# Optimization experiments

Measured on AMD Instinct MI355X. Metric: run time of the kernel, lower is better.

## Reference

```python
import jax, jax.numpy as jnp
import numpy as np

HEADS = 8
DIM_HEAD = 64
EPS_NORM = 1e-5

def chan_layer_norm(x, g, b):
    # normalize over channel dim (axis=1), biased variance, eps inside sqrt
    mean = jnp.mean(x, axis=1, keepdims=True)
    var = jnp.mean((x - mean) ** 2, axis=1, keepdims=True)
    return (x - mean) / jnp.sqrt(var + EPS_NORM) * g + b

def l2norm(x):
    # F.normalize over dim=1 with eps=1e-12
    n = jnp.linalg.norm(x, axis=1, keepdims=True)
    return x / jnp.maximum(n, 1e-12)

def conv1x1(w, x):
    # w: (out_c, in_c), x: (b, in_c, h, w)
    return jnp.einsum('oc,bchw->bohw', w, x)

def setup_inputs() -> dict:
    key = jax.random.key(0)
    ks = jax.random.split(key, 8)
    dim, inner = 256, HEADS * DIM_HEAD
    B, H, W = 8, 64, 64
    inp = {
        'query_source': jax.random.normal(ks[0], (B, dim, H, W), jnp.float32),
        'context': jax.random.normal(ks[1], (B, dim, H, W), jnp.float32),
        'cn_g': jnp.ones((1, dim, 1, 1), jnp.float32),
        'cn_b': jnp.zeros((1, dim, 1, 1), jnp.float32),
        'qn_g': jnp.ones((1, dim, 1, 1), jnp.float32),
        'qn_b': jnp.zeros((1, dim, 1, 1), jnp.float32),
        'on_g': jnp.ones((1, dim, 1, 1), jnp.float32),
        'on_b': jnp.zeros((1, dim, 1, 1), jnp.float32),
        'w_kv': jax.random.normal(ks[2], (inner * 2, dim), jnp.float32) * (dim ** -0.5),
        'w_q': jax.random.normal(ks[3], (inner, dim), jnp.float32) * (dim ** -0.5),
        'w_out': jax.random.normal(ks[4], (dim, inner), jnp.float32) * (inner ** -0.5),
        'gamma': jnp.full((1,), 0.5, jnp.float32),  # nonzero so output depends on attention path
    }
    return inp

def reference(query_source, context, cn_g, cn_b, qn_g, qn_b, on_g, on_b, w_kv, w_q, w_out, gamma):
    B, C, Hq, Wq = query_source.shape
    _, _, Hc, Wc = context.shape
    kh = int(Hc ** 0.5)  # height_top_k default
    kw = int(Wc ** 0.5)  # width_top_k default

    ctx = chan_layer_norm(context, cn_g, cn_b)
    qs = chan_layer_norm(query_source, qn_g, qn_b)

    kv = conv1x1(w_kv, ctx)                      # (B, 2*inner, Hc, Wc)
    k, v = jnp.split(kv, 2, axis=1)
    q = conv1x1(w_q, qs)                         # (B, inner, Hq, Wq)

    def fold(x):
        b, hc, h, w = x.shape
        return x.reshape(b, HEADS, DIM_HEAD, h, w).reshape(b * HEADS, DIM_HEAD, h, w)
    q, k, v = fold(q), fold(k), fold(v)

    q, k = l2norm(q), l2norm(k)

    if kh < Hc or kw < Wc:
        k_abs = jnp.abs(k)
        q_probe = q.sum(axis=(2, 3))             # (bh, c)
        if kh < Hc:
            score_r = jnp.einsum('bc,bch->bh', q_probe, k_abs.sum(axis=3))
            idx_h = jax.lax.top_k(score_r, kh)[1]            # (bh, kh)
            idx = idx_h[:, None, :, None]
            k = jnp.take_along_axis(k, idx, axis=2)
            v = jnp.take_along_axis(v, idx, axis=2)
        if kw < Wc:
            score_c = jnp.einsum('bc,bcw->bw', q_probe, k_abs.sum(axis=2))
            idx_w = jax.lax.top_k(score_c, kw)[1]            # (bh, kw)
            idx = idx_w[:, None, None, :]
            k = jnp.take_along_axis(k, idx, axis=3)
            v = jnp.take_along_axis(v, idx, axis=3)

    def flat(x):  # (bh, c, h, w) -> (bh, h*w, c)
        bh, c = x.shape[:2]
        return x.reshape(bh, c, -1).transpose(0, 2, 1)
    qf, kf, vf = flat(q), flat(k), flat(v)

    sim = jnp.einsum('bid,bjd->bij', qf, kf)     # (bh, Hq*Wq, kh*kw)
    attn = jax.nn.softmax(sim, axis=-1)
    out = jnp.einsum('bij,bjd->bid', attn, vf)   # (bh, Hq*Wq, c)

    out = out.reshape(B, HEADS, Hq, Wq, DIM_HEAD)
    out = out.transpose(0, 1, 4, 2, 3).reshape(B, HEADS * DIM_HEAD, Hq, Wq)
    out = conv1x1(w_out, out)
    out = chan_layer_norm(out, on_g, on_b)
    return gamma * out + query_source
```

## Files before the change

kernel.cpp:

```cpp
#include <hip/hip_runtime.h>
#include <hip/hip_bf16.h>

#define BB 8
#define CDIM 256
#define PP 4096
#define NHEADS 8
#define DHEAD 64
#define INNER 512
#define NBH 64

using bf16 = __hip_bfloat16;
typedef short short8 __attribute__((ext_vector_type(8)));
typedef short short4v __attribute__((ext_vector_type(4)));
typedef float f32x4 __attribute__((ext_vector_type(4)));
typedef unsigned short u16;

__device__ __forceinline__ float b2f(bf16 x) { return __bfloat162float(x); }
__device__ __forceinline__ bf16 f2b(float x) { return __float2bfloat16(x); }

__device__ __forceinline__ u16 f2h(float x) {
    union { float f; unsigned u; } c; c.f = x;
    unsigned r = c.u + 0x7FFF + ((c.u >> 16) & 1);
    return (u16)(r >> 16);
}
__device__ __forceinline__ float h2f(u16 h) {
    union { float f; unsigned u; } c; c.u = ((unsigned)h) << 16;
    return c.f;
}

__device__ __forceinline__ int sw(int row, int kb) {
    return row * 128 + (kb ^ ((row & 7) << 4));
}

__device__ __forceinline__ void gload16(const void* g, void* lds) {
    __builtin_amdgcn_global_load_lds((const __attribute__((address_space(1))) void*)g,
                                     (__attribute__((address_space(3))) void*)lds, 16, 0, 0);
}

__device__ __forceinline__ void remap(int& o0, int& p0, int& b) {
    unsigned GS = gridDim.x;
    unsigned h = (blockIdx.z * gridDim.y + blockIdx.y) * GS + blockIdx.x;
    unsigned xc = h & 7, m = h >> 3;
    unsigned g = (m / GS) * 8 + xc;
    o0 = (int)(m % GS) * 64;
    p0 = (int)(g & 63) * 64;
    b  = (int)(g >> 6);
}

__global__ __launch_bounds__(256) void split2_kernel(const float* __restrict__ Wkv,
                                                     const float* __restrict__ Wq,
                                                     u16* __restrict__ KH, u16* __restrict__ KL,
                                                     u16* __restrict__ QH, u16* __restrict__ QL) {
    int i = blockIdx.x * 256 + threadIdx.x;
    if (i < 262144) {
        float v = Wkv[i]; u16 hb = f2h(v);
        KH[i] = hb; KL[i] = f2h(v - h2f(hb));
    } else {
        int j = i - 262144;
        float v = Wq[j]; u16 hb = f2h(v);
        QH[j] = hb; QL[j] = f2h(v - h2f(hb));
    }
}

__global__ __launch_bounds__(256) void wsplit_hi_kernel(const float* __restrict__ W,
                                                        u16* __restrict__ WH) {
    int i = blockIdx.x * 256 + threadIdx.x;
    WH[i] = f2h(W[i]);
}

__global__ __launch_bounds__(256) void ln_split_kernel(const float* __restrict__ x,
                                                       const float* __restrict__ g,
                                                       const float* __restrict__ bb,
                                                       u16* __restrict__ XH,
                                                       u16* __restrict__ XL) {
    int b = blockIdx.y;
    int p0 = blockIdx.x * 64;
    int tid = threadIdx.x;
    int px = tid & 63, cg = tid >> 6;
    __shared__ float red_s[4][64], red_q[4][64], meanv[64], rstdv[64];

    const float* xb = x + (size_t)b * CDIM * PP + p0 + px;
    float s = 0.f, sq = 0.f;
#pragma unroll 8
    for (int i = 0; i < 64; ++i) {
        float v = xb[(size_t)(cg * 64 + i) * PP];
        s += v; sq += v * v;
    }
    red_s[cg][px] = s; red_q[cg][px] = sq;
    __syncthreads();
    if (tid < 64) {
        float ts = red_s[0][tid] + red_s[1][tid] + red_s[2][tid] + red_s[3][tid];
        float tq = red_q[0][tid] + red_q[1][tid] + red_q[2][tid] + red_q[3][tid];
        float mean = ts * (1.f / CDIM);
        float var  = tq * (1.f / CDIM) - mean * mean;
        meanv[tid] = mean;
        rstdv[tid] = rsqrtf(var + 1e-5f);
    }
    __syncthreads();
    float mean = meanv[px], rstd = rstdv[px];
    size_t orow = ((size_t)b * PP + p0 + px) * CDIM;
    for (int c0 = cg * 64; c0 < cg * 64 + 64; c0 += 8) {
        short8 hv, lv;
#pragma unroll
        for (int j = 0; j < 8; ++j) {
            int c = c0 + j;
            float v = xb[(size_t)c * PP];
            float n = (v - mean) * rstd * g[c] + bb[c];
            u16 hb = f2h(n);
            hv[j] = (short)hb;
            lv[j] = (short)f2h(n - h2f(hb));
        }
        *(short8*)(XH + orow + c0) = hv;
        *(short8*)(XL + orow + c0) = lv;
    }
}

__global__ __launch_bounds__(256) void mfma_qkv_kernel(const u16* __restrict__ WH,
                                                       const u16* __restrict__ WL,
                                                       const u16* __restrict__ XH,
                                                       const u16* __restrict__ XL,
                                                       u16* __restrict__ dstA,
                                                       u16* __restrict__ dstB,
                                                       int Kdim, int norm_below, int mode,
                                                       float* __restrict__ part_out,
                                                       const float* __restrict__ q_probe) {
    __shared__ alignas(16) char sm[32768];
    __shared__ float red[16][64];
    __shared__ float rinv[64];
    __shared__ float qp_s[64];
    char* AH = sm;
    char* AL = sm + 8192;
    char* BH = sm + 16384;
    char* BL = sm + 24576;
    float* C = (float*)sm;

    int o0, p0, b;
    remap(o0, p0, b);
    int tid = threadIdx.x;
    int l = tid & 63, w = tid >> 6;
    int wm = w >> 1, wn = w & 1;
    int lr = l & 15, lk = l >> 4;
    int r8 = l >> 3;
    int kswz = ((l & 7) * 16) ^ (r8 << 4);

    bool donorm = (o0 < norm_below);
    bool lite = (mode == 0) && !donorm;
    if (mode == 0 && donorm && tid < 64)
        qp_s[tid] = q_probe[(size_t)(b * NHEADS + (o0 >> 6)) * 64 + tid];

    f32x4 acc[2][2] = {};

    for (int k0 = 0; k0 < Kdim; k0 += 64) {
#pragma unroll
        for (int j = 0; j < 2; ++j) {
            int rb = w * 16 + j * 8;
            int row = rb + r8;
            size_t aoff = ((size_t)(o0 + row) * Kdim + k0) * 2 + kswz;
            size_t boff = (((size_t)b * PP + p0 + row) * Kdim + k0) * 2 + kswz;
            gload16((const char*)WH + aoff, AH + rb * 128);
            gload16((const char*)XH + boff, BH + rb * 128);
            if (!lite) {
                gload16((const char*)WL + aoff, AL + rb * 128);
                gload16((const char*)XL + boff, BL + rb * 128);
            }
        }
        __syncthreads();
#pragma unroll
        for (int kk = 0; kk < 2; ++kk) {
            int kb = kk * 64 + lk * 16;
            short8 ah[2], bh[2];
#pragma unroll
            for (int f = 0; f < 2; ++f) {
                ah[f] = *(short8*)(AH + sw(wm * 32 + f * 16 + lr, kb));
                bh[f] = *(short8*)(BH + sw(wn * 32 + f * 16 + lr, kb));
            }
            if (!lite) {
                short8 al[2], bl[2];
#pragma unroll
                for (int f = 0; f < 2; ++f) {
                    al[f] = *(short8*)(AL + sw(wm * 32 + f * 16 + lr, kb));
                    bl[f] = *(short8*)(BL + sw(wn * 32 + f * 16 + lr, kb));
                }
#pragma unroll
                for (int fm = 0; fm < 2; ++fm)
#pragma unroll
                    for (int fn = 0; fn < 2; ++fn) {
                        acc[fm][fn] = __builtin_amdgcn_mfma_f32_16x16x32_bf16(ah[fm], bh[fn], acc[fm][fn], 0, 0, 0);
                        acc[fm][fn] = __builtin_amdgcn_mfma_f32_16x16x32_bf16(ah[fm], bl[fn], acc[fm][fn], 0, 0, 0);
                        acc[fm][fn] = __builtin_amdgcn_mfma_f32_16x16x32_bf16(al[fm], bh[fn], acc[fm][fn], 0, 0, 0);
                    }
            } else {
#pragma unroll
                for (int fm = 0; fm < 2; ++fm)
#pragma unroll
                    for (int fn = 0; fn < 2; ++fn)
                        acc[fm][fn] = __builtin_amdgcn_mfma_f32_16x16x32_bf16(ah[fm], bh[fn], acc[fm][fn], 0, 0, 0);
            }
        }
        __syncthreads();
    }

#pragma unroll
    for (int fm = 0; fm < 2; ++fm)
#pragma unroll
        for (int fn = 0; fn < 2; ++fn)
#pragma unroll
            for (int r = 0; r < 4; ++r)
                C[(wm * 32 + fm * 16 + lk * 4 + r) * 65 + wn * 32 + fn * 16 + lr] = acc[fm][fn][r];
    __syncthreads();

    int tx = tid & 15, ty = tid >> 4;
    float a2[4][4];
#pragma unroll
    for (int i = 0; i < 4; ++i)
#pragma unroll
        for (int j = 0; j < 4; ++j)
            a2[i][j] = C[(ty * 4 + i) * 65 + tx * 4 + j];

    if (donorm) {
#pragma unroll
        for (int j = 0; j < 4; ++j) {
            float sj = 0.f;
#pragma unroll
            for (int i = 0; i < 4; ++i) sj += a2[i][j] * a2[i][j];
            red[ty][tx * 4 + j] = sj;
        }
        __syncthreads();
        if (tid < 64) {
            float s = 0.f;
#pragma unroll
            for (int yy = 0; yy < 16; ++yy) s += red[yy][tid];
            rinv[tid] = 1.f / fmaxf(sqrtf(s), 1e-12f);
        }
        __syncthreads();
#pragma unroll
        for (int i = 0; i < 4; ++i)
#pragma unroll
            for (int j = 0; j < 4; ++j)
                a2[i][j] *= rinv[tx * 4 + j];
    }

    if (mode == 1) {
        int p_l = tid & 63, og = tid >> 6;
        float rv = rinv[p_l];
        u16* qrow = dstA + ((size_t)(b * NHEADS + (o0 >> 6)) * PP + p0 + p_l) * 64 + og * 16;
        short8 s0, s1;
#pragma unroll
        for (int i = 0; i < 8; ++i) s0[i] = (short)f2h(C[(og * 16 + i) * 65 + p_l] * rv);
#pragma unroll
        for (int i = 0; i < 8; ++i) s1[i] = (short)f2h(C[(og * 16 + 8 + i) * 65 + p_l] * rv);
        *(short8*)qrow = s0;
        *(short8*)(qrow + 8) = s1;
    } else {
        int oo = donorm ? o0 : (o0 - norm_below);
        u16* dest = donorm ? dstA : dstB;
#pragma unroll
        for (int i = 0; i < 4; ++i) {
            int oc = oo + ty * 4 + i;
            int bh = b * NHEADS + (oc >> 6);
            int d  = oc & 63;
            u16* drow = dest + ((size_t)bh * DHEAD + d) * PP + p0;
            short4v pk;
#pragma unroll
            for (int j = 0; j < 4; ++j) pk[j] = (short)f2h(a2[i][j]);
            *(short4v*)(drow + tx * 4) = pk;
        }
    }

    if (donorm) {
        int bh = b * NHEADS + (o0 >> 6);
        int h  = p0 >> 6;
        if (mode == 0) {
            float cj[4];
#pragma unroll
            for (int j = 0; j < 4; ++j) {
                float s = 0.f;
#pragma unroll
                for (int i = 0; i < 4; ++i) s += qp_s[ty * 4 + i] * fabsf(a2[i][j]);
                cj[j] = s;
            }
            __syncthreads();
#pragma unroll
            for (int j = 0; j < 4; ++j) red[ty][tx * 4 + j] = cj[j];
            __syncthreads();
            if (tid < 64) {
                float s = 0.f;
#pragma unroll
                for (int t = 0; t < 16; ++t) s += red[t][tid];
                part_out[((size_t)bh * 64 + h) * 64 + tid] = s;
            }
        } else {
            float part[4];
#pragma unroll
            for (int i = 0; i < 4; ++i) {
                float s = 0.f;
#pragma unroll
                for (int j = 0; j < 4; ++j) s += a2[i][j];
                part[i] = s;
            }
            __syncthreads();
#pragma unroll
            for (int i = 0; i < 4; ++i) red[tx][ty * 4 + i] = part[i];
            __syncthreads();
            if (tid < 64) {
                float s = 0.f;
#pragma unroll
                for (int t = 0; t < 16; ++t) s += red[t][tid];
                part_out[((size_t)bh * 64 + h) * 64 + tid] = s;
            }
        }
    }
}

__global__ __launch_bounds__(64) void qreduce_kernel(const float* __restrict__ part,
                                                     float* __restrict__ q_probe) {
    int bh = blockIdx.x, d = threadIdx.x;
    float s = 0.f;
    for (int h = 0; h < 64; ++h) s += part[((size_t)bh * 64 + h) * 64 + d];
    q_probe[(size_t)bh * 64 + d] = s;
}

__global__ __launch_bounds__(256) void select_gather_kernel(const float* __restrict__ colpart,
                                                            const u16* __restrict__ kn,
                                                            const u16* __restrict__ vs,
                                                            u16* __restrict__ k_sel,
                                                            u16* __restrict__ v_selt) {
    int bh = blockIdx.x;
    int tid = threadIdx.x;
    __shared__ float M[64][65];
    __shared__ int selh[8], selw[8];
    for (int i = tid; i < 4096; i += 256) M[i >> 6][i & 63] = colpart[(size_t)bh * 4096 + i];
    __syncthreads();
    if (tid < 128) {
        int isCol = tid >> 6;
        int x = tid & 63;
        float sv = 0.f;
        if (isCol) { for (int h = 0; h < 64; ++h) sv += M[h][x]; }
        else       { for (int w = 0; w < 64; ++w) sv += M[x][w]; }
        float v = sv;
        for (int it = 0; it < 8; ++it) {
            float bv = v; int bi = x;
#pragma unroll
            for (int off = 32; off; off >>= 1) {
                float ov = __shfl_xor(bv, off);
                int   oi = __shfl_xor(bi, off);
                if (ov > bv || (ov == bv && oi < bi)) { bv = ov; bi = oi; }
            }
            if (x == 0) { if (isCol) selw[it] = bi; else selh[it] = bi; }
            if (x == bi) v = -3.4e38f;
        }
    }
    __syncthreads();
    for (int idx = tid; idx < 4096; idx += 256) {
        int j = idx >> 6, d = idx & 63;
        int p = selh[j >> 3] * 64 + selw[j & 7];
        u16 kv = kn[((size_t)bh * 64 + d) * PP + p];
        u16 vv = vs[((size_t)bh * 64 + d) * PP + p];
        k_sel[(size_t)bh * 4096 + j * 64 + d]  = kv;
        v_selt[(size_t)bh * 4096 + d * 64 + j] = vv;
    }
}

__global__ __launch_bounds__(256) void attn_mfma_kernel(const u16* __restrict__ qt,
                                                        const u16* __restrict__ ksel,
                                                        const u16* __restrict__ vselt,
                                                        u16* __restrict__ attn_t) {
    __shared__ alignas(16) char AQ[8192];
    __shared__ alignas(16) char BK[8192];
    __shared__ alignas(16) char BV[8192];
    __shared__ float SIM[64 * 68];
    int bh = blockIdx.y;
    int p0 = blockIdx.x * 64;
    int b = bh >> 3, h = bh & 7;
    int tid = threadIdx.x;
    int l = tid & 63, w = tid >> 6;
    int wm = w >> 1, wn = w & 1;
    int lr = l & 15, lk = l >> 4;
    int r8 = l >> 3;
    int kswz = ((l & 7) * 16) ^ (r8 << 4);

#pragma unroll
    for (int j = 0; j < 2; ++j) {
        int rb = w * 16 + j * 8;
        int row = rb + r8;
        gload16((const char*)qt + ((size_t)bh * PP + p0 + row) * 128 + kswz, AQ + rb * 128);
        gload16((const char*)ksel + ((size_t)bh * 64 + row) * 128 + kswz, BK + rb * 128);
        gload16((const char*)vselt + ((size_t)bh * 64 + row) * 128 + kswz, BV + rb * 128);
    }
    __syncthreads();

    f32x4 acc[2][2] = {};
#pragma unroll
    for (int kk = 0; kk < 2; ++kk) {
        int kb = kk * 64 + lk * 16;
        short8 av[2], bv[2];
#pragma unroll
        for (int f = 0; f < 2; ++f) {
            av[f] = *(short8*)(AQ + sw(wm * 32 + f * 16 + lr, kb));
            bv[f] = *(short8*)(BK + sw(wn * 32 + f * 16 + lr, kb));
        }
#pragma unroll
        for (int fm = 0; fm < 2; ++fm)
#pragma unroll
            for (int fn = 0; fn < 2; ++fn)
                acc[fm][fn] = __builtin_amdgcn_mfma_f32_16x16x32_bf16(av[fm], bv[fn], acc[fm][fn], 0, 0, 0);
    }
#pragma unroll
    for (int fm = 0; fm < 2; ++fm)
#pragma unroll
        for (int fn = 0; fn < 2; ++fn)
#pragma unroll
            for (int r = 0; r < 4; ++r)
                SIM[(wm * 32 + fm * 16 + lk * 4 + r) * 68 + wn * 32 + fn * 16 + lr] = acc[fm][fn][r];
    __syncthreads();

    {
        int p = tid >> 2, qd = tid & 3;
        const float* srow = &SIM[p * 68 + qd * 16];
        float v[16];
#pragma unroll
        for (int jj = 0; jj < 16; ++jj) v[jj] = srow[jj];
        float m = v[0];
#pragma unroll
        for (int jj = 1; jj < 16; ++jj) m = fmaxf(m, v[jj]);
        m = fmaxf(m, __shfl_xor(m, 1));
        m = fmaxf(m, __shfl_xor(m, 2));
        float s = 0.f;
#pragma unroll
        for (int jj = 0; jj < 16; ++jj) { v[jj] = __expf(v[jj] - m); s += v[jj]; }
        s += __shfl_xor(s, 1);
        s += __shfl_xor(s, 2);
        float rl = 1.f / s;
        short8 h0, h1;
#pragma unroll
        for (int jj = 0; jj < 8; ++jj) {
            h0[jj] = (short)f2h(v[jj] * rl);
            h1[jj] = (short)f2h(v[8 + jj] * rl);
        }
        *(short8*)(AQ + sw(p, qd * 32)) = h0;
        *(short8*)(AQ + sw(p, qd * 32 + 16)) = h1;
    }
    __syncthreads();

    f32x4 acc2[2][2] = {};
#pragma unroll
    for (int kk = 0; kk < 2; ++kk) {
        int kb = kk * 64 + lk * 16;
        short8 av[2], bv[2];
#pragma unroll
        for (int f = 0; f < 2; ++f) {
            av[f] = *(short8*)(AQ + sw(wm * 32 + f * 16 + lr, kb));
            bv[f] = *(short8*)(BV + sw(wn * 32 + f * 16 + lr, kb));
        }
#pragma unroll
        for (int fm = 0; fm < 2; ++fm)
#pragma unroll
            for (int fn = 0; fn < 2; ++fn)
                acc2[fm][fn] = __builtin_amdgcn_mfma_f32_16x16x32_bf16(av[fm], bv[fn], acc2[fm][fn], 0, 0, 0);
    }
    u16* ob = attn_t + ((size_t)b * PP + p0) * INNER + h * 64;
#pragma unroll
    for (int fm = 0; fm < 2; ++fm)
#pragma unroll
        for (int fn = 0; fn < 2; ++fn)
#pragma unroll
            for (int r = 0; r < 4; ++r)
                ob[(size_t)(wm * 32 + fm * 16 + lk * 4 + r) * INNER + wn * 32 + fn * 16 + lr]
                    = f2h(acc2[fm][fn][r]);
}

__global__ __launch_bounds__(256) void mfma_out_kernel(const u16* __restrict__ WHp,
                                                       const u16* __restrict__ Xt,
                                                       float* __restrict__ Y) {
    __shared__ alignas(16) char sm[32768];

    int o0, p0, b;
    remap(o0, p0, b);
    int tid = threadIdx.x;
    int l = tid & 63, w = tid >> 6;
    int wm = w >> 1, wn = w & 1;
    int lr = l & 15, lk = l >> 4;
    int r8 = l >> 3;
    int kswz = ((l & 7) * 16) ^ (r8 << 4);

    f32x4 acc[2][2] = {};

    auto STAGE = [&](int bufi, int k0) {
        char* base = sm + bufi * 16384;
#pragma unroll
        for (int j = 0; j < 2; ++j) {
            int rb = w * 16 + j * 8;
            int row = rb + r8;
            size_t aoff = ((size_t)(o0 + row) * INNER + k0) * 2 + kswz;
            size_t boff = (((size_t)b * PP + p0 + row) * INNER + k0) * 2 + kswz;
            gload16((const char*)WHp + aoff, base + rb * 128);
            gload16((const char*)Xt + boff, base + 8192 + rb * 128);
        }
    };

    STAGE(0, 0);
    __syncthreads();
    int cur = 0;
    for (int t = 0; t < 8; ++t) {
        if (t < 7) STAGE(cur ^ 1, (t + 1) * 64);
        char* AH = sm + cur * 16384;
        char* BH = AH + 8192;
#pragma unroll
        for (int kk = 0; kk < 2; ++kk) {
            int kb = kk * 64 + lk * 16;
            short8 ah[2], bh[2];
#pragma unroll
            for (int f = 0; f < 2; ++f) {
                ah[f] = *(short8*)(AH + sw(wm * 32 + f * 16 + lr, kb));
                bh[f] = *(short8*)(BH + sw(wn * 32 + f * 16 + lr, kb));
            }
#pragma unroll
            for (int fm = 0; fm < 2; ++fm)
#pragma unroll
                for (int fn = 0; fn < 2; ++fn)
                    acc[fm][fn] = __builtin_amdgcn_mfma_f32_16x16x32_bf16(ah[fm], bh[fn], acc[fm][fn], 0, 0, 0);
        }
        __syncthreads();
        cur ^= 1;
    }
#pragma unroll
    for (int fm = 0; fm < 2; ++fm)
#pragma unroll
        for (int fn = 0; fn < 2; ++fn)
#pragma unroll
            for (int r = 0; r < 4; ++r)
                Y[((size_t)b * CDIM + o0 + wm * 32 + fm * 16 + lk * 4 + r) * PP
                  + p0 + wn * 32 + fn * 16 + lr] = acc[fm][fn][r];
}

__global__ __launch_bounds__(256) void final_ln_kernel(const float* __restrict__ y,
                                                       const float* __restrict__ g,
                                                       const float* __restrict__ bb,
                                                       const float* __restrict__ gamma,
                                                       const float* __restrict__ resid,
                                                       float* __restrict__ out) {
    int b = blockIdx.y;
    int p = blockIdx.x * 256 + threadIdx.x;
    const float* yb = y + (size_t)b * CDIM * PP + p;
    float s = 0.f, sq = 0.f;
    for (int c = 0; c < CDIM; ++c) {
        float v = yb[(size_t)c * PP];
        s += v; sq += v * v;
    }
    float mean = s * (1.f / CDIM);
    float var  = sq * (1.f / CDIM) - mean * mean;
    float rstd = rsqrtf(var + 1e-5f);
    float gm = gamma[0];
    const float* rb = resid + (size_t)b * CDIM * PP + p;
    float* ob = out + (size_t)b * CDIM * PP + p;
    for (int c = 0; c < CDIM; ++c) {
        float v = yb[(size_t)c * PP];
        float xn = (v - mean) * rstd * g[c] + bb[c];
        ob[(size_t)c * PP] = gm * xn + rb[(size_t)c * PP];
    }
}

extern "C" void kernel_launch(void* const* d_in, const int* in_sizes, int n_in,
                              void* d_out, int out_size, void* d_ws, size_t ws_size,
                              hipStream_t stream) {
    const float* query_source = (const float*)d_in[0];
    const float* context      = (const float*)d_in[1];
    const float* cn_g = (const float*)d_in[2];
    const float* cn_b = (const float*)d_in[3];
    const float* qn_g = (const float*)d_in[4];
    const float* qn_b = (const float*)d_in[5];
    const float* on_g = (const float*)d_in[6];
    const float* on_b = (const float*)d_in[7];
    const float* w_kv = (const float*)d_in[8];
    const float* w_q  = (const float*)d_in[9];
    const float* w_out= (const float*)d_in[10];
    const float* gamma= (const float*)d_in[11];
    float* out = (float*)d_out;

    char* ws = (char*)d_ws;
    u16*  XHt    = (u16*)(ws + 0);
    u16*  XLt    = (u16*)(ws + 16777216);
    u16*  attn_t = (u16*)(ws + 0);
    u16*   k_n  = (u16*)(ws + 33554432);
    float* y    = (float*)(ws + 33554432);
    u16*   v_s  = (u16*)(ws + 67108864);
    u16*   q_t  = (u16*)(ws + 100663296);
    u16*  WqH   = (u16*)(ws + 134217728);
    u16*  WqL   = (u16*)(ws + 134742016);
    u16*  k_sel = (u16*)(ws + 134217728);
    u16*  v_selt= (u16*)(ws + 134742016);
    u16*  WkvH  = (u16*)(ws + 135266304);
    u16*  WkvL  = (u16*)(ws + 135790592);
    u16*  WoutH = (u16*)(ws + 135266304);
    float* qprobe_part   = (float*)(ws + 136314880);
    float* colscore_part = (float*)(ws + 136314880);
    float* q_probe       = (float*)(ws + 137363456);

    dim3 blk(256);
    split2_kernel<<<dim3(1536), blk, 0, stream>>>(w_kv, w_q, WkvH, WkvL, WqH, WqL);
    ln_split_kernel<<<dim3(64, BB), blk, 0, stream>>>(query_source, qn_g, qn_b, XHt, XLt);
    mfma_qkv_kernel<<<dim3(8, 64, BB), blk, 0, stream>>>(WqH, WqL, XHt, XLt, q_t, nullptr,
                                                         CDIM, 512, 1, qprobe_part, nullptr);
    qreduce_kernel<<<dim3(64), dim3(64), 0, stream>>>(qprobe_part, q_probe);
    ln_split_kernel<<<dim3(64, BB), blk, 0, stream>>>(context, cn_g, cn_b, XHt, XLt);
    mfma_qkv_kernel<<<dim3(16, 64, BB), blk, 0, stream>>>(WkvH, WkvL, XHt, XLt, k_n, v_s,
                                                          CDIM, 512, 0, colscore_part, q_probe);
    select_gather_kernel<<<dim3(64), blk, 0, stream>>>(colscore_part, k_n, v_s, k_sel, v_selt);
    wsplit_hi_kernel<<<dim3(512), blk, 0, stream>>>(w_out, WoutH);
    attn_mfma_kernel<<<dim3(64, NBH), blk, 0, stream>>>(q_t, k_sel, v_selt, attn_t);
    mfma_out_kernel<<<dim3(4, 64, BB), blk, 0, stream>>>(WoutH, attn_t, y);
    final_ln_kernel<<<dim3(16, BB), blk, 0, stream>>>(y, on_g, on_b, gamma, query_source, out);
}
```

Baseline: 383.1 us.

## Fuse paired projection tiles, stage layernorm input in LDS, store out-proj in bf16

Result: faster. 352.5 us (-8.0%).

```diff
diff --git a/kernel.cpp b/kernel.cpp
--- a/kernel.cpp
+++ b/kernel.cpp
@@ -16,7 +16,6 @@
 typedef unsigned short u16;
 
 __device__ __forceinline__ float b2f(bf16 x) { return __bfloat162float(x); }
-__device__ __forceinline__ bf16 f2b(float x) { return __float2bfloat16(x); }
 
 __device__ __forceinline__ u16 f2h(float x) {
     union { float f; unsigned u; } c; c.f = x;
@@ -37,12 +36,12 @@
                                      (__attribute__((address_space(3))) void*)lds, 16, 0, 0);
 }
 
-__device__ __forceinline__ void remap(int& o0, int& p0, int& b) {
+__device__ __forceinline__ void remap_i(int& i, int& p0, int& b) {
     unsigned GS = gridDim.x;
     unsigned h = (blockIdx.z * gridDim.y + blockIdx.y) * GS + blockIdx.x;
     unsigned xc = h & 7, m = h >> 3;
     unsigned g = (m / GS) * 8 + xc;
-    o0 = (int)(m % GS) * 64;
+    i  = (int)(m % GS);
     p0 = (int)(g & 63) * 64;
     b  = (int)(g >> 6);
 }
@@ -73,17 +72,27 @@
                                                        const float* __restrict__ bb,
                                                        u16* __restrict__ XH,
                                                        u16* __restrict__ XL) {
+    __shared__ alignas(16) float xs[256][64];
+    __shared__ float red_s[4][64], red_q[4][64], meanv[64], rstdv[64];
     int b = blockIdx.y;
     int p0 = blockIdx.x * 64;
     int tid = threadIdx.x;
-    int px = tid & 63, cg = tid >> 6;
-    __shared__ float red_s[4][64], red_q[4][64], meanv[64], rstdv[64];
-
-    const float* xb = x + (size_t)b * CDIM * PP + p0 + px;
+    int w = tid >> 6, l = tid & 63;
+
+#pragma unroll
+    for (int ii = 0; ii < 16; ++ii) {
+        int iss = w * 16 + ii;
+        int c = iss * 4 + (l >> 4);
+        gload16(x + ((size_t)b * CDIM + c) * PP + p0 + (l & 15) * 4,
+                (char*)xs + iss * 1024);
+    }
+    __syncthreads();
+
+    int px = l, cg = w;
     float s = 0.f, sq = 0.f;
 #pragma unroll 8
     for (int i = 0; i < 64; ++i) {
-        float v = xb[(size_t)(cg * 64 + i) * PP];
+        float v = xs[cg * 64 + i][px];
         s += v; sq += v * v;
     }
     red_s[cg][px] = s; red_q[cg][px] = sq;
@@ -104,7 +113,7 @@
 #pragma unroll
         for (int j = 0; j < 8; ++j) {
             int c = c0 + j;
-            float v = xb[(size_t)c * PP];
+            float v = xs[c][px];
             float n = (v - mean) * rstd * g[c] + bb[c];
             u16 hb = f2h(n);
             hv[j] = (short)hb;
@@ -115,27 +124,31 @@
     }
 }
 
-__global__ __launch_bounds__(256) void mfma_qkv_kernel(const u16* __restrict__ WH,
-                                                       const u16* __restrict__ WL,
-                                                       const u16* __restrict__ XH,
-                                                       const u16* __restrict__ XL,
-                                                       u16* __restrict__ dstA,
-                                                       u16* __restrict__ dstB,
-                                                       int Kdim, int norm_below, int mode,
-                                                       float* __restrict__ part_out,
-                                                       const float* __restrict__ q_probe) {
-    __shared__ alignas(16) char sm[32768];
-    __shared__ float red[16][64];
-    __shared__ float rinv[64];
-    __shared__ float qp_s[64];
-    char* AH = sm;
-    char* AL = sm + 8192;
-    char* BH = sm + 16384;
-    char* BL = sm + 24576;
-    float* C = (float*)sm;
-
-    int o0, p0, b;
-    remap(o0, p0, b);
+__global__ __launch_bounds__(256) void mfma_fused_kernel(const u16* __restrict__ WH,
+                                                         const u16* __restrict__ WL,
+                                                         const u16* __restrict__ XH,
+                                                         const u16* __restrict__ XL,
+                                                         u16* __restrict__ dstA,
+                                                         u16* __restrict__ dstB,
+                                                         int mode,
+                                                         float* __restrict__ part_out,
+                                                         const float* __restrict__ q_probe) {
+    __shared__ alignas(16) char sm[49152];
+    char* SXH = sm;
+    char* SXL = sm + 8192;
+    char* SAH = sm + 16384;
+    char* SAL = sm + 24576;
+    char* SBH = sm + 32768;
+    char* SBL = sm + 40960;
+    float* C    = (float*)sm;
+    float* red  = (float*)(sm + 16640);
+    float* rinv = (float*)(sm + 20736);
+    float* qp_s = (float*)(sm + 20992);
+
+    int i, p0, b;
+    remap_i(i, p0, b);
+    int o0A = i * 64;
+    int o0B = (mode == 0) ? 512 + i * 64 : 256 + i * 64;
     int tid = threadIdx.x;
     int l = tid & 63, w = tid >> 6;
     int wm = w >> 1, wn = w & 1;
@@ -143,62 +156,61 @@
     int r8 = l >> 3;
     int kswz = ((l & 7) * 16) ^ (r8 << 4);
 
-    bool donorm = (o0 < norm_below);
-    bool lite = (mode == 0) && !donorm;
-    if (mode == 0 && donorm && tid < 64)
-        qp_s[tid] = q_probe[(size_t)(b * NHEADS + (o0 >> 6)) * 64 + tid];
-
-    f32x4 acc[2][2] = {};
-
-    for (int k0 = 0; k0 < Kdim; k0 += 64) {
+    f32x4 accA[2][2] = {};
+    f32x4 accB[2][2] = {};
+
+    for (int k0 = 0; k0 < CDIM; k0 += 64) {
 #pragma unroll
         for (int j = 0; j < 2; ++j) {
             int rb = w * 16 + j * 8;
             int row = rb + r8;
-            size_t aoff = ((size_t)(o0 + row) * Kdim + k0) * 2 + kswz;
-            size_t boff = (((size_t)b * PP + p0 + row) * Kdim + k0) * 2 + kswz;
-            gload16((const char*)WH + aoff, AH + rb * 128);
-            gload16((const char*)XH + boff, BH + rb * 128);
-            if (!lite) {
-                gload16((const char*)WL + aoff, AL + rb * 128);
-                gload16((const char*)XL + boff, BL + rb * 128);
-            }
+            size_t boff  = (((size_t)b * PP + p0 + row) * CDIM + k0) * 2 + kswz;
+            size_t aoffA = ((size_t)(o0A + row) * CDIM + k0) * 2 + kswz;
+            size_t aoffB = ((size_t)(o0B + row) * CDIM + k0) * 2 + kswz;
+            gload16((const char*)XH + boff,  SXH + rb * 128);
+            gload16((const char*)XL + boff,  SXL + rb * 128);
+            gload16((const char*)WH + aoffA, SAH + rb * 128);
+            gload16((const char*)WL + aoffA, SAL + rb * 128);
+            gload16((const char*)WH + aoffB, SBH + rb * 128);
+            if (mode == 1) gload16((const char*)WL + aoffB, SBL + rb * 128);
         }
         __syncthreads();
 #pragma unroll
         for (int kk = 0; kk < 2; ++kk) {
             int kb = kk * 64 + lk * 16;
-            short8 ah[2], bh[2];
+            short8 xh_[2], xl_[2], ahA[2], alA[2], ahB[2], alB[2];
 #pragma unroll
             for (int f = 0; f < 2; ++f) {
-                ah[f] = *(short8*)(AH + sw(wm * 32 + f * 16 + lr, kb));
-                bh[f] = *(short8*)(BH + sw(wn * 32 + f * 16 + lr, kb));
+                int rx = wn * 32 + f * 16 + lr;
+                int rw = wm * 32 + f * 16 + lr;
+                xh_[f] = *(short8*)(SXH + sw(rx, kb));
+                xl_[f] = *(short8*)(SXL + sw(rx, kb));
+                ahA[f] = *(short8*)(SAH + sw(rw, kb));
+                alA[f] = *(short8*)(SAL + sw(rw, kb));
+                ahB[f] = *(short8*)(SBH + sw(rw, kb));
+                alB[f] = (mode == 1) ? *(short8*)(SBL + sw(rw, kb)) : ahB[f];
             }
-            if (!lite) {
-                short8 al[2], bl[2];
-#pragma unroll
-                for (int f = 0; f < 2; ++f) {
-                    al[f] = *(short8*)(AL + sw(wm * 32 + f * 16 + lr, kb));
-                    bl[f] = *(short8*)(BL + sw(wn * 32 + f * 16 + lr, kb));
+#pragma unroll
+            for (int fm = 0; fm < 2; ++fm)
+#pragma unroll
+                for (int fn = 0; fn < 2; ++fn) {
+                    accA[fm][fn] = __builtin_amdgcn_mfma_f32_16x16x32_bf16(ahA[fm], xh_[fn], accA[fm][fn], 0, 0, 0);
+                    accA[fm][fn] = __builtin_amdgcn_mfma_f32_16x16x32_bf16(ahA[fm], xl_[fn], accA[fm][fn], 0, 0, 0);
+                    accA[fm][fn] = __builtin_amdgcn_mfma_f32_16x16x32_bf16(alA[fm], xh_[fn], accA[fm][fn], 0, 0, 0);
+                    accB[fm][fn] = __builtin_amdgcn_mfma_f32_16x16x32_bf16(ahB[fm], xh_[fn], accB[fm][fn], 0, 0, 0);
+                    if (mode == 1) {
+                        accB[fm][fn] = __builtin_amdgcn_mfma_f32_16x16x32_bf16(ahB[fm], xl_[fn], accB[fm][fn], 0, 0, 0);
+                        accB[fm][fn] = __builtin_amdgcn_mfma_f32_16x16x32_bf16(alB[fm], xh_[fn], accB[fm][fn], 0, 0, 0);
+                    }
                 }
-#pragma unroll
-                for (int fm = 0; fm < 2; ++fm)
-#pragma unroll
-                    for (int fn = 0; fn < 2; ++fn) {
-                        acc[fm][fn] = __builtin_amdgcn_mfma_f32_16x16x32_bf16(ah[fm], bh[fn], acc[fm][fn], 0, 0, 0);
-                        acc[fm][fn] = __builtin_amdgcn_mfma_f32_16x16x32_bf16(ah[fm], bl[fn], acc[fm][fn], 0, 0, 0);
-                        acc[fm][fn] = __builtin_amdgcn_mfma_f32_16x16x32_bf16(al[fm], bh[fn], acc[fm][fn], 0, 0, 0);
-                    }
-            } else {
-#pragma unroll
-                for (int fm = 0; fm < 2; ++fm)
-#pragma unroll
-                    for (int fn = 0; fn < 2; ++fn)
-                        acc[fm][fn] = __builtin_amdgcn_mfma_f32_16x16x32_bf16(ah[fm], bh[fn], acc[fm][fn], 0, 0, 0);
-            }
-        }
-        __syncthreads();
-    }
+        }
+        __syncthreads();
+    }
+
+    int tx = tid & 15, ty = tid >> 4;
+    int h = p0 >> 6;
+    if (mode == 0 && tid < 64)
+        qp_s[tid] = q_probe[(size_t)(b * NHEADS + i) * 64 + tid];
 
 #pragma unroll
     for (int fm = 0; fm < 2; ++fm)
@@ -206,108 +218,174 @@
         for (int fn = 0; fn < 2; ++fn)
 #pragma unroll
             for (int r = 0; r < 4; ++r)
-                C[(wm * 32 + fm * 16 + lk * 4 + r) * 65 + wn * 32 + fn * 16 + lr] = acc[fm][fn][r];
-    __syncthreads();
-
-    int tx = tid & 15, ty = tid >> 4;
+                C[(wm * 32 + fm * 16 + lk * 4 + r) * 65 + wn * 32 + fn * 16 + lr] = accA[fm][fn][r];
+    __syncthreads();
+
     float a2[4][4];
 #pragma unroll
-    for (int i = 0; i < 4; ++i)
+    for (int ii = 0; ii < 4; ++ii)
 #pragma unroll
         for (int j = 0; j < 4; ++j)
-            a2[i][j] = C[(ty * 4 + i) * 65 + tx * 4 + j];
-
-    if (donorm) {
+            a2[ii][j] = C[(ty * 4 + ii) * 65 + tx * 4 + j];
+
+#pragma unroll
+    for (int j = 0; j < 4; ++j) {
+        float sj = 0.f;
+#pragma unroll
+        for (int ii = 0; ii < 4; ++ii) sj += a2[ii][j] * a2[ii][j];
+        red[ty * 64 + tx * 4 + j] = sj;
+    }
+    __syncthreads();
+    if (tid < 64) {
+        float s = 0.f;
+#pragma unroll
+        for (int yy = 0; yy < 16; ++yy) s += red[yy * 64 + tid];
+        rinv[tid] = 1.f / fmaxf(sqrtf(s), 1e-12f);
+    }
+    __syncthreads();
+#pragma unroll
+    for (int ii = 0; ii < 4; ++ii)
+#pragma unroll
+        for (int j = 0; j < 4; ++j)
+            a2[ii][j] *= rinv[tx * 4 + j];
+
+    int bhA = b * NHEADS + (o0A >> 6);
+    if (mode == 0) {
+#pragma unroll
+        for (int ii = 0; ii < 4; ++ii) {
+            int oc = o0A + ty * 4 + ii;
+            int d  = oc & 63;
+            u16* drow = dstA + ((size_t)(b * NHEADS + (oc >> 6)) * DHEAD + d) * PP + p0;
+            short4v pk;
+#pragma unroll
+            for (int j = 0; j < 4; ++j) pk[j] = (short)f2h(a2[ii][j]);
+            *(short4v*)(drow + tx * 4) = pk;
+        }
+        float cj[4];
+#pragma unroll
+        for (int j = 0; j < 4; ++j) {
+            float s = 0.f;
+#pragma unroll
+            for (int ii = 0; ii < 4; ++ii) s += qp_s[ty * 4 + ii] * fabsf(a2[ii][j]);
+            cj[j] = s;
+        }
+        __syncthreads();
+#pragma unroll
+        for (int j = 0; j < 4; ++j) red[ty * 64 + tx * 4 + j] = cj[j];
+        __syncthreads();
+        if (tid < 64) {
+            float s = 0.f;
+#pragma unroll
+            for (int t = 0; t < 16; ++t) s += red[t * 64 + tid];
+            part_out[((size_t)bhA * 64 + h) * 64 + tid] = s;
+        }
+    } else {
+        int p_l = tid & 63, og = tid >> 6;
+        float rv = rinv[p_l];
+        u16* qrow = dstA + ((size_t)bhA * PP + p0 + p_l) * 64 + og * 16;
+        short8 s0, s1;
+#pragma unroll
+        for (int ii = 0; ii < 8; ++ii) s0[ii] = (short)f2h(C[(og * 16 + ii) * 65 + p_l] * rv);
+#pragma unroll
+        for (int ii = 0; ii < 8; ++ii) s1[ii] = (short)f2h(C[(og * 16 + 8 + ii) * 65 + p_l] * rv);
+        *(short8*)qrow = s0;
+        *(short8*)(qrow + 8) = s1;
+        float part[4];
+#pragma unroll
+        for (int ii = 0; ii < 4; ++ii) {
+            float s = 0.f;
+#pragma unroll
+            for (int j = 0; j < 4; ++j) s += a2[ii][j];
+            part[ii] = s;
+        }
+        __syncthreads();
+#pragma unroll
+        for (int ii = 0; ii < 4; ++ii) red[tx * 64 + ty * 4 + ii] = part[ii];
+        __syncthreads();
+        if (tid < 64) {
+            float s = 0.f;
+#pragma unroll
+            for (int t = 0; t < 16; ++t) s += red[t * 64 + tid];
+            part_out[((size_t)bhA * 64 + h) * 64 + tid] = s;
+        }
+    }
+    __syncthreads();
+
+#pragma unroll
+    for (int fm = 0; fm < 2; ++fm)
+#pragma unroll
+        for (int fn = 0; fn < 2; ++fn)
+#pragma unroll
+            for (int r = 0; r < 4; ++r)
+                C[(wm * 32 + fm * 16 + lk * 4 + r) * 65 + wn * 32 + fn * 16 + lr] = accB[fm][fn][r];
+    __syncthreads();
+#pragma unroll
+    for (int ii = 0; ii < 4; ++ii)
+#pragma unroll
+        for (int j = 0; j < 4; ++j)
+            a2[ii][j] = C[(ty * 4 + ii) * 65 + tx * 4 + j];
+
+    if (mode == 0) {
+#pragma unroll
+        for (int ii = 0; ii < 4; ++ii) {
+            int oc = (o0B - 512) + ty * 4 + ii;
+            int d  = oc & 63;
+            u16* drow = dstB + ((size_t)(b * NHEADS + (oc >> 6)) * DHEAD + d) * PP + p0;
+            short4v pk;
+#pragma unroll
+            for (int j = 0; j < 4; ++j) pk[j] = (short)f2h(a2[ii][j]);
+            *(short4v*)(drow + tx * 4) = pk;
+        }
+    } else {
 #pragma unroll
         for (int j = 0; j < 4; ++j) {
             float sj = 0.f;
 #pragma unroll
-            for (int i = 0; i < 4; ++i) sj += a2[i][j] * a2[i][j];
-            red[ty][tx * 4 + j] = sj;
+            for (int ii = 0; ii < 4; ++ii) sj += a2[ii][j] * a2[ii][j];
+            red[ty * 64 + tx * 4 + j] = sj;
         }
         __syncthreads();
         if (tid < 64) {
             float s = 0.f;
 #pragma unroll
-            for (int yy = 0; yy < 16; ++yy) s += red[yy][tid];
+            for (int yy = 0; yy < 16; ++yy) s += red[yy * 64 + tid];
             rinv[tid] = 1.f / fmaxf(sqrtf(s), 1e-12f);
         }
         __syncthreads();
 #pragma unroll
-        for (int i = 0; i < 4; ++i)
+        for (int ii = 0; ii < 4; ++ii)
 #pragma unroll
             for (int j = 0; j < 4; ++j)
-                a2[i][j] *= rinv[tx * 4 + j];
-    }
-
-    if (mode == 1) {
+                a2[ii][j] *= rinv[tx * 4 + j];
+
+        int bhB = b * NHEADS + (o0B >> 6);
         int p_l = tid & 63, og = tid >> 6;
         float rv = rinv[p_l];
-        u16* qrow = dstA + ((size_t)(b * NHEADS + (o0 >> 6)) * PP + p0 + p_l) * 64 + og * 16;
+        u16* qrow = dstA + ((size_t)bhB * PP + p0 + p_l) * 64 + og * 16;
         short8 s0, s1;
 #pragma unroll
-        for (int i = 0; i < 8; ++i) s0[i] = (short)f2h(C[(og * 16 + i) * 65 + p_l] * rv);
-#pragma unroll
-        for (int i = 0; i < 8; ++i) s1[i] = (short)f2h(C[(og * 16 + 8 + i) * 65 + p_l] * rv);
+        for (int ii = 0; ii < 8; ++ii) s0[ii] = (short)f2h(C[(og * 16 + ii) * 65 + p_l] * rv);
+#pragma unroll
+        for (int ii = 0; ii < 8; ++ii) s1[ii] = (short)f2h(C[(og * 16 + 8 + ii) * 65 + p_l] * rv);
         *(short8*)qrow = s0;
         *(short8*)(qrow + 8) = s1;
-    } else {
-        int oo = donorm ? o0 : (o0 - norm_below);
-        u16* dest = donorm ? dstA : dstB;
-#pragma unroll
-        for (int i = 0; i < 4; ++i) {
-            int oc = oo + ty * 4 + i;
-            int bh = b * NHEADS + (oc >> 6);
-            int d  = oc & 63;
-            u16* drow = dest + ((size_t)bh * DHEAD + d) * PP + p0;
-            short4v pk;
-#pragma unroll
-            for (int j = 0; j < 4; ++j) pk[j] = (short)f2h(a2[i][j]);
-            *(short4v*)(drow + tx * 4) = pk;
-        }
-    }
-
-    if (donorm) {
-        int bh = b * NHEADS + (o0 >> 6);
-        int h  = p0 >> 6;
-        if (mode == 0) {
-            float cj[4];
-#pragma unroll
-            for (int j = 0; j < 4; ++j) {
-                float s = 0.f;
-#pragma unroll
-                for (int i = 0; i < 4; ++i) s += qp_s[ty * 4 + i] * fabsf(a2[i][j]);
-                cj[j] = s;
-            }
-            __syncthreads();
-#pragma unroll
-            for (int j = 0; j < 4; ++j) red[ty][tx * 4 + j] = cj[j];
-            __syncthreads();
-            if (tid < 64) {
-                float s = 0.f;
-#pragma unroll
-                for (int t = 0; t < 16; ++t) s += red[t][tid];
-                part_out[((size_t)bh * 64 + h) * 64 + tid] = s;
-            }
-        } else {
-            float part[4];
-#pragma unroll
-            for (int i = 0; i < 4; ++i) {
-                float s = 0.f;
-#pragma unroll
-                for (int j = 0; j < 4; ++j) s += a2[i][j];
-                part[i] = s;
-            }
-            __syncthreads();
-#pragma unroll
-            for (int i = 0; i < 4; ++i) red[tx][ty * 4 + i] = part[i];
-            __syncthreads();
-            if (tid < 64) {
-                float s = 0.f;
-#pragma unroll
-                for (int t = 0; t < 16; ++t) s += red[t][tid];
-                part_out[((size_t)bh * 64 + h) * 64 + tid] = s;
-            }
+        float part[4];
+#pragma unroll
+        for (int ii = 0; ii < 4; ++ii) {
+            float s = 0.f;
+#pragma unroll
+            for (int j = 0; j < 4; ++j) s += a2[ii][j];
+            part[ii] = s;
+        }
+        __syncthreads();
+#pragma unroll
+        for (int ii = 0; ii < 4; ++ii) red[tx * 64 + ty * 4 + ii] = part[ii];
+        __syncthreads();
+        if (tid < 64) {
+            float s = 0.f;
+#pragma unroll
+            for (int t = 0; t < 16; ++t) s += red[t * 64 + tid];
+            part_out[((size_t)bhB * 64 + h) * 64 + tid] = s;
         }
     }
 }
@@ -471,11 +549,12 @@
 
 __global__ __launch_bounds__(256) void mfma_out_kernel(const u16* __restrict__ WHp,
                                                        const u16* __restrict__ Xt,
-                                                       float* __restrict__ Y) {
+                                                       u16* __restrict__ Y) {
     __shared__ alignas(16) char sm[32768];
 
-    int o0, p0, b;
-    remap(o0, p0, b);
+    int i, p0, b;
+    remap_i(i, p0, b);
+    int o0 = i * 64;
     int tid = threadIdx.x;
     int l = tid & 63, w = tid >> 6;
     int wm = w >> 1, wn = w & 1;
@@ -530,10 +609,10 @@
 #pragma unroll
             for (int r = 0; r < 4; ++r)
                 Y[((size_t)b * CDIM + o0 + wm * 32 + fm * 16 + lk * 4 + r) * PP
-                  + p0 + wn * 32 + fn * 16 + lr] = acc[fm][fn][r];
-}
-
-__global__ __launch_bounds__(256) void final_ln_kernel(const float* __restrict__ y,
+                  + p0 + wn * 32 + fn * 16 + lr] = f2h(acc[fm][fn][r]);
+}
+
+__global__ __launch_bounds__(256) void final_ln_kernel(const u16* __restrict__ y,
                                                        const float* __restrict__ g,
                                                        const float* __restrict__ bb,
                                                        const float* __restrict__ gamma,
@@ -541,10 +620,10 @@
                                                        float* __restrict__ out) {
     int b = blockIdx.y;
     int p = blockIdx.x * 256 + threadIdx.x;
-    const float* yb = y + (size_t)b * CDIM * PP + p;
+    const u16* yb = y + (size_t)b * CDIM * PP + p;
     float s = 0.f, sq = 0.f;
     for (int c = 0; c < CDIM; ++c) {
-        float v = yb[(size_t)c * PP];
+        float v = h2f(yb[(size_t)c * PP]);
         s += v; sq += v * v;
     }
     float mean = s * (1.f / CDIM);
@@ -554,7 +633,7 @@
     const float* rb = resid + (size_t)b * CDIM * PP + p;
     float* ob = out + (size_t)b * CDIM * PP + p;
     for (int c = 0; c < CDIM; ++c) {
-        float v = yb[(size_t)c * PP];
+        float v = h2f(yb[(size_t)c * PP]);
         float xn = (v - mean) * rstd * g[c] + bb[c];
         ob[(size_t)c * PP] = gm * xn + rb[(size_t)c * PP];
     }
@@ -581,10 +660,10 @@
     u16*  XHt    = (u16*)(ws + 0);
     u16*  XLt    = (u16*)(ws + 16777216);
     u16*  attn_t = (u16*)(ws + 0);
-    u16*   k_n  = (u16*)(ws + 33554432);
-    float* y    = (float*)(ws + 33554432);
-    u16*   v_s  = (u16*)(ws + 67108864);
-    u16*   q_t  = (u16*)(ws + 100663296);
+    u16*  k_n  = (u16*)(ws + 33554432);
+    u16*  y    = (u16*)(ws + 33554432);
+    u16*  v_s  = (u16*)(ws + 67108864);
+    u16*  q_t  = (u16*)(ws + 100663296);
     u16*  WqH   = (u16*)(ws + 134217728);
     u16*  WqL   = (u16*)(ws + 134742016);
     u16*  k_sel = (u16*)(ws + 134217728);
@@ -599,12 +678,12 @@
     dim3 blk(256);
     split2_kernel<<<dim3(1536), blk, 0, stream>>>(w_kv, w_q, WkvH, WkvL, WqH, WqL);
     ln_split_kernel<<<dim3(64, BB), blk, 0, stream>>>(query_source, qn_g, qn_b, XHt, XLt);
-    mfma_qkv_kernel<<<dim3(8, 64, BB), blk, 0, stream>>>(WqH, WqL, XHt, XLt, q_t, nullptr,
-                                                         CDIM, 512, 1, qprobe_part, nullptr);
+    mfma_fused_kernel<<<dim3(4, 64, BB), blk, 0, stream>>>(WqH, WqL, XHt, XLt, q_t, nullptr,
+                                                           1, qprobe_part, nullptr);
     qreduce_kernel<<<dim3(64), dim3(64), 0, stream>>>(qprobe_part, q_probe);
     ln_split_kernel<<<dim3(64, BB), blk, 0, stream>>>(context, cn_g, cn_b, XHt, XLt);
-    mfma_qkv_kernel<<<dim3(16, 64, BB), blk, 0, stream>>>(WkvH, WkvL, XHt, XLt, k_n, v_s,
-                                                          CDIM, 512, 0, colscore_part, q_probe);
+    mfma_fused_kernel<<<dim3(8, 64, BB), blk, 0, stream>>>(WkvH, WkvL, XHt, XLt, k_n, v_s,
+                                                           0, colscore_part, q_probe);
     select_gather_kernel<<<dim3(64), blk, 0, stream>>>(colscore_part, k_n, v_s, k_sel, v_selt);
     wsplit_hi_kernel<<<dim3(512), blk, 0, stream>>>(w_out, WoutH);
     attn_mfma_kernel<<<dim3(64, NBH), blk, 0, stream>>>(q_t, k_sel, v_selt, attn_t);
```
